# Optimization experiments

Measured on AMD Instinct MI355X. Metric: run time of the kernel, lower is better.

## Reference

```python
import jax, jax.numpy as jnp
import numpy as np

N_NODES = 50000
N_EDGES = 800000
FEAT = 128

def setup_inputs() -> dict:
    key = jax.random.key(0)
    k1, k2, k3, k4 = jax.random.split(key, 4)
    layer_input = jax.random.normal(k1, (N_NODES, FEAT), dtype=jnp.float32)
    # learned edge weights, init uniform(0,1) as in nn.init.uniform_
    w = jax.random.uniform(k2, (N_EDGES,), dtype=jnp.float32)
    row = jax.random.randint(k3, (N_EDGES,), 0, N_NODES, dtype=jnp.int32)
    col = jax.random.randint(k4, (N_EDGES,), 0, N_NODES, dtype=jnp.int32)
    return {"layer_input": layer_input, "w": w, "row": row, "col": col}

def reference(layer_input, w, row, col):
    # sparse.mm(adj, layer_input): adj[row[e], col[e]] = w[e]
    # x[i, f] = sum_{e: row[e]==i} w[e] * layer_input[col[e], f]
    msgs = w[:, None] * layer_input[col]                         # [E, F] gather + scale
    x = jax.ops.segment_sum(msgs, row, num_segments=N_NODES)     # [N, F] scatter-add
    x = jax.nn.relu(x)
    # mm(ones[out_dim, N], x)[0][0] == sum over nodes of column 0 of x
    return jax.nn.sigmoid(jnp.sum(x[:, 0]))
```

## Files before the change

### kernel.cpp

```cpp
#include <hip/hip_runtime.h>

#define N_NODES 50000
#define N_EDGES 800000
#define FEAT    128

#define NRANGE  4
#define RBLKS   64
#define RNODES  (N_NODES / NRANGE)
#define SLICE_Q (N_EDGES / RBLKS / 4)
#define TB      1024


__global__ void pack_zero(const float* __restrict__ li,
                          float* __restrict__ li0,
                          float* __restrict__ sum,
                          unsigned* __restrict__ ticket) {
    int i = blockIdx.x * blockDim.x + threadIdx.x;
    if (i < N_NODES) li0[i] = li[(long)i * FEAT];
    if (i == 0) { *sum = 0.0f; *ticket = 0u; }
}


__global__ __launch_bounds__(TB) void range_accum(
        const float* __restrict__ li0,
        const float* __restrict__ w,
        const int* __restrict__ row,
        const int* __restrict__ col,
        float* __restrict__ partial) {
    __shared__ float accl[RNODES];
    const int r  = blockIdx.x & (NRANGE - 1);
    const int s  = blockIdx.x >> 2;
    const int lo = r * RNODES;

    for (int i = threadIdx.x; i < RNODES; i += TB) accl[i] = 0.0f;
    __syncthreads();

    const float4* wq = (const float4*)w   + (size_t)s * SLICE_Q;
    const int4*   rq = (const int4*)row   + (size_t)s * SLICE_Q;
    const int4*   cq = (const int4*)col   + (size_t)s * SLICE_Q;

    for (int q = threadIdx.x; q < SLICE_Q; q += TB) {
        float4 wv = wq[q];
        int4   rv = rq[q];
        int4   cv = cq[q];
        int a;
        a = rv.x - lo; if ((unsigned)a < RNODES) atomicAdd(&accl[a], wv.x * li0[cv.x]);
        a = rv.y - lo; if ((unsigned)a < RNODES) atomicAdd(&accl[a], wv.y * li0[cv.y]);
        a = rv.z - lo; if ((unsigned)a < RNODES) atomicAdd(&accl[a], wv.z * li0[cv.z]);
        a = rv.w - lo; if ((unsigned)a < RNODES) atomicAdd(&accl[a], wv.w * li0[cv.w]);
    }
    __syncthreads();

    float4* pdst = (float4*)(partial + (size_t)blockIdx.x * RNODES);
    const float4* psrc = (const float4*)accl;
    for (int i = threadIdx.x; i < RNODES / 4; i += TB) pdst[i] = psrc[i];
}

__global__ void reduce_fin(const float* __restrict__ partial,
                           float* __restrict__ sum,
                           unsigned* __restrict__ ticket,
                           float* __restrict__ out) {
    int g = blockIdx.x * blockDim.x + threadIdx.x;
    float local = 0.0f;
    if (g < N_NODES / 4) {
        int r  = g / (RNODES / 4);
        int gl = g - r * (RNODES / 4);
        const float4* base = (const float4*)(partial + (size_t)r * RBLKS * RNODES) + gl;
        float ax = 0.0f, ay = 0.0f, az = 0.0f, aw = 0.0f;
        #pragma unroll 8
        for (int b = 0; b < RBLKS; ++b) {
            float4 p = base[(size_t)b * (RNODES / 4)];
            ax += p.x; ay += p.y; az += p.z; aw += p.w;
        }
        local = fmaxf(ax, 0.0f) + fmaxf(ay, 0.0f) +
                fmaxf(az, 0.0f) + fmaxf(aw, 0.0f);
    }
    #pragma unroll
    for (int off = 32; off > 0; off >>= 1)
        local += __shfl_down(local, off, 64);
    __shared__ float sm[4];
    int wid = threadIdx.x >> 6;
    if ((threadIdx.x & 63) == 0) sm[wid] = local;
    __syncthreads();
    if (threadIdx.x == 0) {
        atomicAdd(sum, sm[0] + sm[1] + sm[2] + sm[3]);
        __threadfence();
        unsigned old = atomicAdd(ticket, 1u);
        if (old == gridDim.x - 1) {
            __threadfence();
            float v = *(volatile float*)sum;
            out[0] = 1.0f / (1.0f + expf(-v));
        }
    }
}


__global__ void zero_acc(float* __restrict__ acc) {
    int i = blockIdx.x * blockDim.x + threadIdx.x;
    if (i < N_NODES) acc[i] = 0.0f;
}

__global__ void edge_scatter4(const float* __restrict__ li0,
                              const float* __restrict__ w,
                              const int* __restrict__ row,
                              const int* __restrict__ col,
                              float* __restrict__ acc) {
    int t = blockIdx.x * blockDim.x + threadIdx.x;
    if (t < N_EDGES / 4) {
        float4 wv = ((const float4*)w)[t];
        int4   rv = ((const int4*)row)[t];
        int4   cv = ((const int4*)col)[t];
        atomicAdd(&acc[rv.x], wv.x * li0[cv.x]);
        atomicAdd(&acc[rv.y], wv.y * li0[cv.y]);
        atomicAdd(&acc[rv.z], wv.z * li0[cv.z]);
        atomicAdd(&acc[rv.w], wv.w * li0[cv.w]);
    }
}

__global__ void relu_sum_fin(const float* __restrict__ acc,
                             float* __restrict__ sum,
                             unsigned* __restrict__ ticket,
                             float* __restrict__ out) {
    float local = 0.0f;
    for (int i = blockIdx.x * blockDim.x + threadIdx.x; i < N_NODES / 4;
         i += gridDim.x * blockDim.x) {
        float4 a = ((const float4*)acc)[i];
        local += fmaxf(a.x, 0.0f) + fmaxf(a.y, 0.0f) +
                 fmaxf(a.z, 0.0f) + fmaxf(a.w, 0.0f);
    }
    #pragma unroll
    for (int off = 32; off > 0; off >>= 1)
        local += __shfl_down(local, off, 64);
    __shared__ float sm[4];
    int wid = threadIdx.x >> 6;
    if ((threadIdx.x & 63) == 0) sm[wid] = local;
    __syncthreads();
    if (threadIdx.x == 0) {
        atomicAdd(sum, sm[0] + sm[1] + sm[2] + sm[3]);
        __threadfence();
        unsigned old = atomicAdd(ticket, 1u);
        if (old == gridDim.x - 1) {
            __threadfence();
            float v = *(volatile float*)sum;
            out[0] = 1.0f / (1.0f + expf(-v));
        }
    }
}

extern "C" void kernel_launch(void* const* d_in, const int* in_sizes, int n_in,
                              void* d_out, int out_size, void* d_ws, size_t ws_size,
                              hipStream_t stream) {
    const float* li  = (const float*)d_in[0];
    const float* w   = (const float*)d_in[1];
    const int*   row = (const int*)d_in[2];
    const int*   col = (const int*)d_in[3];
    float* out = (float*)d_out;

    size_t need = (size_t)N_NODES * 4
                + (size_t)NRANGE * RBLKS * RNODES * 4
                + 16;

    if (ws_size >= need) {
        float*    li0     = (float*)d_ws;
        float*    partial = li0 + N_NODES;
        float*    sum     = partial + (size_t)NRANGE * RBLKS * RNODES;
        unsigned* ticket  = (unsigned*)(sum + 1);

        pack_zero<<<(N_NODES + 255) / 256, 256, 0, stream>>>(li, li0, sum, ticket);
        range_accum<<<NRANGE * RBLKS, TB, 0, stream>>>(li0, w, row, col, partial);
        reduce_fin<<<(N_NODES / 4 + 255) / 256, 256, 0, stream>>>(partial, sum, ticket, out);
    } else {
        float*    acc    = (float*)d_ws;
        float*    li0    = acc + N_NODES;
        float*    sum    = li0 + N_NODES;
        unsigned* ticket = (unsigned*)(sum + 1);

        pack_zero<<<(N_NODES + 255) / 256, 256, 0, stream>>>(li, li0, sum, ticket);
        zero_acc<<<(N_NODES + 255) / 256, 256, 0, stream>>>(acc);
        edge_scatter4<<<(N_EDGES / 4 + 255) / 256, 256, 0, stream>>>(li0, w, row, col, acc);
        relu_sum_fin<<<49, 256, 0, stream>>>(acc, sum, ticket, out);
    }
}
```

Baseline: 29.49 us.

## Fuse edge accumulation and reduction into one kernel with a grid barrier

Drops the separate column-0 packing kernel and gathers layer_input[col*128] directly in the edge loop. Merges the range accumulation and the final reduce into one kernel, joined by a global atomic spin barrier, with 16-lane teams summing the 64 slice partials. The aim is to cut launch overhead and the extra pass that writes and reads li0. The cost is strided uncached gathers into the 25.6MB input and reliance on all 256 blocks of 1024 threads being co-resident, or the barrier deadlocks.

```diff
diff --git a/kernel.cpp b/kernel.cpp
--- a/kernel.cpp
+++ b/kernel.cpp
@@ -5,34 +5,37 @@
 #define FEAT    128
 
 #define NRANGE  4
-#define RBLKS   64
+#define NSLICE  64
+#define NBLK    (NRANGE * NSLICE)
 #define RNODES  (N_NODES / NRANGE)
-#define SLICE_Q (N_EDGES / RBLKS / 4)
+#define RGROUPS (RNODES / 4)
+#define NGROUPS (N_NODES / 4)
+#define GPB     ((NGROUPS + NBLK - 1) / NBLK)
+#define SLICE_Q (N_EDGES / NSLICE / 4)
 #define TB      1024
 
 
-__global__ void pack_zero(const float* __restrict__ li,
-                          float* __restrict__ li0,
-                          float* __restrict__ sum,
-                          unsigned* __restrict__ ticket) {
-    int i = blockIdx.x * blockDim.x + threadIdx.x;
-    if (i < N_NODES) li0[i] = li[(long)i * FEAT];
-    if (i == 0) { *sum = 0.0f; *ticket = 0u; }
+__global__ void init_ctl(float* sum, unsigned* bar, unsigned* ticket) {
+    *sum = 0.0f; *bar = 0u; *ticket = 0u;
 }
 
-
-__global__ __launch_bounds__(TB) void range_accum(
-        const float* __restrict__ li0,
+__global__ __launch_bounds__(TB) void fused(
+        const float* __restrict__ li,
         const float* __restrict__ w,
         const int* __restrict__ row,
         const int* __restrict__ col,
-        float* __restrict__ partial) {
+        float* __restrict__ partial,
+        float* sum, unsigned* bar, unsigned* ticket,
+        float* __restrict__ out) {
     __shared__ float accl[RNODES];
-    const int r  = blockIdx.x & (NRANGE - 1);
-    const int s  = blockIdx.x >> 2;
+    __shared__ float smr[TB / 64];
+    const int s  = blockIdx.x & (NSLICE - 1);
+    const int r  = blockIdx.x >> 6;
     const int lo = r * RNODES;
 
-    for (int i = threadIdx.x; i < RNODES; i += TB) accl[i] = 0.0f;
+    float4* az = (float4*)accl;
+    for (int i = threadIdx.x; i < RGROUPS; i += TB)
+        az[i] = make_float4(0.f, 0.f, 0.f, 0.f);
     __syncthreads();
 
     const float4* wq = (const float4*)w   + (size_t)s * SLICE_Q;
@@ -44,63 +47,78 @@
         int4   rv = rq[q];
         int4   cv = cq[q];
         int a;
-        a = rv.x - lo; if ((unsigned)a < RNODES) atomicAdd(&accl[a], wv.x * li0[cv.x]);
-        a = rv.y - lo; if ((unsigned)a < RNODES) atomicAdd(&accl[a], wv.y * li0[cv.y]);
-        a = rv.z - lo; if ((unsigned)a < RNODES) atomicAdd(&accl[a], wv.z * li0[cv.z]);
-        a = rv.w - lo; if ((unsigned)a < RNODES) atomicAdd(&accl[a], wv.w * li0[cv.w]);
+        a = rv.x - lo; if ((unsigned)a < RNODES) atomicAdd(&accl[a], wv.x * li[(size_t)cv.x * FEAT]);
+        a = rv.y - lo; if ((unsigned)a < RNODES) atomicAdd(&accl[a], wv.y * li[(size_t)cv.y * FEAT]);
+        a = rv.z - lo; if ((unsigned)a < RNODES) atomicAdd(&accl[a], wv.z * li[(size_t)cv.z * FEAT]);
+        a = rv.w - lo; if ((unsigned)a < RNODES) atomicAdd(&accl[a], wv.w * li[(size_t)cv.w * FEAT]);
     }
     __syncthreads();
 
     float4* pdst = (float4*)(partial + (size_t)blockIdx.x * RNODES);
-    const float4* psrc = (const float4*)accl;
-    for (int i = threadIdx.x; i < RNODES / 4; i += TB) pdst[i] = psrc[i];
-}
+    for (int i = threadIdx.x; i < RGROUPS; i += TB) pdst[i] = az[i];
 
-__global__ void reduce_fin(const float* __restrict__ partial,
-                           float* __restrict__ sum,
-                           unsigned* __restrict__ ticket,
-                           float* __restrict__ out) {
-    int g = blockIdx.x * blockDim.x + threadIdx.x;
+    __syncthreads();
+    if (threadIdx.x == 0) {
+        __threadfence();
+        atomicAdd(bar, 1u);
+        while (__hip_atomic_load(bar, __ATOMIC_RELAXED, __HIP_MEMORY_SCOPE_AGENT) < NBLK)
+            __builtin_amdgcn_s_sleep(2);
+    }
+    __syncthreads();
+    __threadfence();
+
+    const int team = threadIdx.x >> 4;
+    const int ln   = threadIdx.x & 15;
     float local = 0.0f;
-    if (g < N_NODES / 4) {
-        int r  = g / (RNODES / 4);
-        int gl = g - r * (RNODES / 4);
-        const float4* base = (const float4*)(partial + (size_t)r * RBLKS * RNODES) + gl;
-        float ax = 0.0f, ay = 0.0f, az = 0.0f, aw = 0.0f;
-        #pragma unroll 8
-        for (int b = 0; b < RBLKS; ++b) {
-            float4 p = base[(size_t)b * (RNODES / 4)];
-            ax += p.x; ay += p.y; az += p.z; aw += p.w;
+    int g = blockIdx.x * GPB + team;
+    if (team < GPB && g < NGROUPS) {
+        int rr = g / RGROUPS;
+        int gl = g - rr * RGROUPS;
+        const float4* base = (const float4*)(partial + (size_t)(rr * NSLICE) * RNODES) + gl;
+        float ax = 0.f, ay = 0.f, az4 = 0.f, aw = 0.f;
+        #pragma unroll
+        for (int pb = 0; pb < 4; ++pb) {
+            float4 p = base[(size_t)(ln + pb * 16) * RGROUPS];
+            ax += p.x; ay += p.y; az4 += p.z; aw += p.w;
         }
-        local = fmaxf(ax, 0.0f) + fmaxf(ay, 0.0f) +
-                fmaxf(az, 0.0f) + fmaxf(aw, 0.0f);
+        #pragma unroll
+        for (int d = 8; d > 0; d >>= 1) {
+            ax  += __shfl_down(ax,  d, 16);
+            ay  += __shfl_down(ay,  d, 16);
+            az4 += __shfl_down(az4, d, 16);
+            aw  += __shfl_down(aw,  d, 16);
+        }
+        if (ln == 0)
+            local = fmaxf(ax, 0.f) + fmaxf(ay, 0.f) +
+                    fmaxf(az4, 0.f) + fmaxf(aw, 0.f);
     }
     #pragma unroll
     for (int off = 32; off > 0; off >>= 1)
         local += __shfl_down(local, off, 64);
-    __shared__ float sm[4];
-    int wid = threadIdx.x >> 6;
-    if ((threadIdx.x & 63) == 0) sm[wid] = local;
+    if ((threadIdx.x & 63) == 0) smr[threadIdx.x >> 6] = local;
     __syncthreads();
     if (threadIdx.x == 0) {
-        atomicAdd(sum, sm[0] + sm[1] + sm[2] + sm[3]);
+        float t = 0.f;
+        #pragma unroll
+        for (int i = 0; i < TB / 64; ++i) t += smr[i];
+        atomicAdd(sum, t);
         __threadfence();
         unsigned old = atomicAdd(ticket, 1u);
-        if (old == gridDim.x - 1) {
-            __threadfence();
-            float v = *(volatile float*)sum;
+        if (old == NBLK - 1) {
+            float v = __hip_atomic_load(sum, __ATOMIC_RELAXED, __HIP_MEMORY_SCOPE_AGENT);
             out[0] = 1.0f / (1.0f + expf(-v));
         }
     }
 }
 
 
-__global__ void zero_acc(float* __restrict__ acc) {
+__global__ void zero_acc(float* __restrict__ acc, float* sum, unsigned* ticket) {
     int i = blockIdx.x * blockDim.x + threadIdx.x;
     if (i < N_NODES) acc[i] = 0.0f;
+    if (i == 0) { *sum = 0.0f; *ticket = 0u; }
 }
 
-__global__ void edge_scatter4(const float* __restrict__ li0,
+__global__ void edge_scatter4(const float* __restrict__ li,
                               const float* __restrict__ w,
                               const int* __restrict__ row,
                               const int* __restrict__ col,
@@ -110,10 +128,10 @@
         float4 wv = ((const float4*)w)[t];
         int4   rv = ((const int4*)row)[t];
         int4   cv = ((const int4*)col)[t];
-        atomicAdd(&acc[rv.x], wv.x * li0[cv.x]);
-        atomicAdd(&acc[rv.y], wv.y * li0[cv.y]);
-        atomicAdd(&acc[rv.z], wv.z * li0[cv.z]);
-        atomicAdd(&acc[rv.w], wv.w * li0[cv.w]);
+        atomicAdd(&acc[rv.x], wv.x * li[(size_t)cv.x * FEAT]);
+        atomicAdd(&acc[rv.y], wv.y * li[(size_t)cv.y * FEAT]);
+        atomicAdd(&acc[rv.z], wv.z * li[(size_t)cv.z * FEAT]);
+        atomicAdd(&acc[rv.w], wv.w * li[(size_t)cv.w * FEAT]);
     }
 }
 
@@ -125,23 +143,21 @@
     for (int i = blockIdx.x * blockDim.x + threadIdx.x; i < N_NODES / 4;
          i += gridDim.x * blockDim.x) {
         float4 a = ((const float4*)acc)[i];
-        local += fmaxf(a.x, 0.0f) + fmaxf(a.y, 0.0f) +
-                 fmaxf(a.z, 0.0f) + fmaxf(a.w, 0.0f);
+        local += fmaxf(a.x, 0.f) + fmaxf(a.y, 0.f) +
+                 fmaxf(a.z, 0.f) + fmaxf(a.w, 0.f);
     }
     #pragma unroll
     for (int off = 32; off > 0; off >>= 1)
         local += __shfl_down(local, off, 64);
     __shared__ float sm[4];
-    int wid = threadIdx.x >> 6;
-    if ((threadIdx.x & 63) == 0) sm[wid] = local;
+    if ((threadIdx.x & 63) == 0) sm[threadIdx.x >> 6] = local;
     __syncthreads();
     if (threadIdx.x == 0) {
         atomicAdd(sum, sm[0] + sm[1] + sm[2] + sm[3]);
         __threadfence();
         unsigned old = atomicAdd(ticket, 1u);
         if (old == gridDim.x - 1) {
-            __threadfence();
-            float v = *(volatile float*)sum;
+            float v = __hip_atomic_load(sum, __ATOMIC_RELAXED, __HIP_MEMORY_SCOPE_AGENT);
             out[0] = 1.0f / (1.0f + expf(-v));
         }
     }
@@ -156,28 +172,23 @@
     const int*   col = (const int*)d_in[3];
     float* out = (float*)d_out;
 
-    size_t need = (size_t)N_NODES * 4
-                + (size_t)NRANGE * RBLKS * RNODES * 4
-                + 16;
+    size_t need = (size_t)NBLK * RNODES * 4 + 16;
 
     if (ws_size >= need) {
-        float*    li0     = (float*)d_ws;
-        float*    partial = li0 + N_NODES;
-        float*    sum     = partial + (size_t)NRANGE * RBLKS * RNODES;
-        unsigned* ticket  = (unsigned*)(sum + 1);
+        float*    partial = (float*)d_ws;
+        float*    sum     = partial + (size_t)NBLK * RNODES;
+        unsigned* bar     = (unsigned*)(sum + 1);
+        unsigned* ticket  = bar + 1;
 
-        pack_zero<<<(N_NODES + 255) / 256, 256, 0, stream>>>(li, li0, sum, ticket);
-        range_accum<<<NRANGE * RBLKS, TB, 0, stream>>>(li0, w, row, col, partial);
-        reduce_fin<<<(N_NODES / 4 + 255) / 256, 256, 0, stream>>>(partial, sum, ticket, out);
+        init_ctl<<<1, 1, 0, stream>>>(sum, bar, ticket);
+        fused<<<NBLK, TB, 0, stream>>>(li, w, row, col, partial, sum, bar, ticket, out);
     } else {
         float*    acc    = (float*)d_ws;
-        float*    li0    = acc + N_NODES;
-        float*    sum    = li0 + N_NODES;
+        float*    sum    = acc + N_NODES;
         unsigned* ticket = (unsigned*)(sum + 1);
 
-        pack_zero<<<(N_NODES + 255) / 256, 256, 0, stream>>>(li, li0, sum, ticket);
-        zero_acc<<<(N_NODES + 255) / 256, 256, 0, stream>>>(acc);
-        edge_scatter4<<<(N_EDGES / 4 + 255) / 256, 256, 0, stream>>>(li0, w, row, col, acc);
+        zero_acc<<<(N_NODES + 255) / 256, 256, 0, stream>>>(acc, sum, ticket);
+        edge_scatter4<<<(N_EDGES / 4 + 255) / 256, 256, 0, stream>>>(li, w, row, col, acc);
         relu_sum_fin<<<49, 256, 0, stream>>>(acc, sum, ticket, out);
     }
 }
```

Result: slower. 112.6 us (+281.9%).
